# Kernel tuning notes

Measured on AMD Instinct MI355X. Metric: run time of the kernel, lower is better.

## Reference

```python
import jax, jax.numpy as jnp
import numpy as np

D = 256
H1, H2 = 256, 128

def setup_inputs() -> dict:
    key0 = jax.random.key(0)
    ks = jax.random.split(key0, 10)
    B, Lq, Lk = 2, 512, 512
    query = jax.random.normal(ks[0], (B, Lq, D), dtype=jnp.float32)
    key_t = jax.random.normal(ks[1], (B, Lk, D), dtype=jnp.float32)
    value = jax.random.normal(ks[2], (B, Lk, D), dtype=jnp.float32)
    mask = jnp.ones((B, Lq, Lk), dtype=jnp.int32)
    s1 = 1.0 / np.sqrt(2 * D)
    W1 = jax.random.uniform(ks[3], (2 * D, H1), jnp.float32, -s1, s1)  # torch Linear(2D,H1), [in,out]
    b1 = jax.random.uniform(ks[4], (H1,), jnp.float32, -s1, s1)
    s2 = 1.0 / np.sqrt(H1)
    W2 = jax.random.uniform(ks[5], (H1, H2), jnp.float32, -s2, s2)
    b2 = jax.random.uniform(ks[6], (H2,), jnp.float32, -s2, s2)
    s3 = 1.0 / np.sqrt(H2)
    W3 = jax.random.uniform(ks[7], (H2, 1), jnp.float32, -s3, s3)
    b3 = jax.random.uniform(ks[8], (1,), jnp.float32, -s3, s3)
    return {"query": query, "key": key_t, "value": value, "mask": mask,
            "W1": W1, "b1": b1, "W2": W2, "b2": b2, "W3": W3, "b3": b3}

def reference(query, key, value, mask, W1, b1, W2, b2, W3, b3):
    # Original: cat([q_i, k_j]) @ W1 == q_i @ W1[:D] + k_j @ W1[D:]  (algebraic split,
    # identical math, avoids materializing the [B,Lq,Lk,2D] concat tensor).
    W1q, W1k = W1[:D], W1[D:]
    qp = jnp.einsum('bqd,dh->bqh', query, W1q)           # [B,Lq,H1]
    kp = jnp.einsum('bkd,dh->bkh', key, W1k)             # [B,Lk,H1]
    h1 = jax.nn.relu(qp[:, :, None, :] + kp[:, None, :, :] + b1)   # [B,Lq,Lk,H1]
    h2 = jax.nn.relu(jnp.einsum('bqkh,hj->bqkj', h1, W2) + b2)      # [B,Lq,Lk,H2]
    scores = (jnp.einsum('bqkj,jo->bqko', h2, W3) + b3)[..., 0]     # [B,Lq,Lk]
    scores = jnp.where(mask == 0, jnp.float32(-1e9), scores)
    attn = jax.nn.softmax(scores, axis=-1)               # dropout is identity in eval mode
    out = jnp.einsum('bqk,bkd->bqd', attn, value)
    return out, attn
```

## Files before the change

### kernel.cpp

```cpp
#include <hip/hip_runtime.h>

#define D_  256
#define H1_ 256
#define H2_ 128
#define B_  2
#define LQ_ 512
#define LK_ 512
#define BK  64

typedef float  f32x4  __attribute__((ext_vector_type(4)));
typedef __bf16 bf16x8 __attribute__((ext_vector_type(8)));
typedef __bf16 bf16x4 __attribute__((ext_vector_type(4)));

__global__ __launch_bounds__(512) void prep_kernel(
    const float* __restrict__ query, const float* __restrict__ key,
    const float* __restrict__ W1, const float* __restrict__ b1,
    const float* __restrict__ W2,
    float* __restrict__ qp, float* __restrict__ kp, __bf16* __restrict__ w2t) {
  const int blk = blockIdx.x;
  const int tid = threadIdx.x;
  if (blk >= 256) {
    const int id = (blk - 256) * 512 + tid;
    const int n = id >> 8;
    const int k = id & 255;
    w2t[n * H1_ + k] = (__bf16)W2[k * H2_ + n];
    return;
  }
  __shared__ float in_lds[8][D_];
  __shared__ float part[8][H1_];
  const int row0 = blk * 8;
  const int sel  = row0 >> 10;
  const float* __restrict__ src = sel ? key : query;
  const int base = (row0 & 1023) * D_;
  for (int i = tid; i < 8 * D_; i += 512)
    in_lds[i >> 8][i & 255] = src[base + i];
  __syncthreads();
  const int h  = tid & 255;
  const int kh = tid >> 8;
  float acc[8] = {0.f, 0.f, 0.f, 0.f, 0.f, 0.f, 0.f, 0.f};
  const float* __restrict__ w = W1 + sel * D_ * H1_ + kh * 128 * H1_ + h;
#pragma unroll 4
  for (int dd = 0; dd < 128; ++dd) {
    const float wv = w[dd * H1_];
    const int d = kh * 128 + dd;
#pragma unroll
    for (int r = 0; r < 8; ++r) acc[r] += in_lds[r][d] * wv;
  }
  if (kh == 1) {
#pragma unroll
    for (int r = 0; r < 8; ++r) part[r][h] = acc[r];
  }
  __syncthreads();
  if (kh == 0) {
    const float bias = sel ? 0.0f : b1[h];
    float* __restrict__ dst = sel ? kp : qp;
#pragma unroll
    for (int r = 0; r < 8; ++r)
      dst[base + r * H1_ + h] = acc[r] + part[r][h] + bias;
  }
}

__global__ __launch_bounds__(256, 2) void score_kernel(
    const float* __restrict__ qp, const float* __restrict__ kp,
    const __bf16* __restrict__ w2t,
    const float* __restrict__ b2, const float* __restrict__ W3,
    const float* __restrict__ b3, float* __restrict__ scores) {
  __shared__ __bf16 A_lds[128][BK + 8];
  __shared__ __bf16 B_lds[128][BK + 8];
  __shared__ float  spart[2][128];

  const int b  = blockIdx.z;
  const int q0 = blockIdx.y * 8;
  const int k0 = blockIdx.x * 16;
  const int tid  = threadIdx.x;
  const int wave = tid >> 6;
  const int lane = tid & 63;
  const int quad = lane >> 4;
  const int l16  = lane & 15;
  const int wm   = wave >> 1;
  const int wn   = wave & 1;

  const float* __restrict__ qpb = qp + (b * LQ_ + q0) * H1_;
  const float* __restrict__ kpb = kp + (b * LK_ + k0) * H1_;

  f32x4 acc[4][4];
#pragma unroll
  for (int mt = 0; mt < 4; ++mt)
#pragma unroll
    for (int nt = 0; nt < 4; ++nt)
      acc[mt][nt] = (f32x4){0.f, 0.f, 0.f, 0.f};

  for (int kc = 0; kc < H1_ / BK; ++kc) {
#pragma unroll
    for (int i = 0; i < 8; ++i) {
      const int r  = i * 16 + (tid >> 4);
      const int kg = tid & 15;
      const int qi = r >> 4, ki = r & 15;
      const int kcol = kc * BK + kg * 4;
      const float4 qv = *(const float4*)(qpb + qi * H1_ + kcol);
      const float4 kv = *(const float4*)(kpb + ki * H1_ + kcol);
      bf16x4 a;
      a[0] = (__bf16)fmaxf(qv.x + kv.x, 0.f);
      a[1] = (__bf16)fmaxf(qv.y + kv.y, 0.f);
      a[2] = (__bf16)fmaxf(qv.z + kv.z, 0.f);
      a[3] = (__bf16)fmaxf(qv.w + kv.w, 0.f);
      *(bf16x4*)(&A_lds[r][kg * 4]) = a;
    }
#pragma unroll
    for (int i = 0; i < 4; ++i) {
      const int u = i * 256 + tid;
      const int n = u >> 3, seg = u & 7;
      *(uint4*)(&B_lds[n][seg * 8]) =
          *(const uint4*)(w2t + n * H1_ + kc * BK + seg * 8);
    }
    __syncthreads();
#pragma unroll
    for (int ks = 0; ks < BK / 32; ++ks) {
      bf16x8 af[4], bfr[4];
#pragma unroll
      for (int mt = 0; mt < 4; ++mt)
        af[mt] = *(const bf16x8*)(&A_lds[wm * 64 + mt * 16 + l16][ks * 32 + quad * 8]);
#pragma unroll
      for (int nt = 0; nt < 4; ++nt)
        bfr[nt] = *(const bf16x8*)(&B_lds[wn * 64 + nt * 16 + l16][ks * 32 + quad * 8]);
#pragma unroll
      for (int mt = 0; mt < 4; ++mt)
#pragma unroll
        for (int nt = 0; nt < 4; ++nt)
          acc[mt][nt] = __builtin_amdgcn_mfma_f32_16x16x32_bf16(
              af[mt], bfr[nt], acc[mt][nt], 0, 0, 0);
    }
    __syncthreads();
  }

  float part[4][4];
#pragma unroll
  for (int mt = 0; mt < 4; ++mt)
#pragma unroll
    for (int rg = 0; rg < 4; ++rg) part[mt][rg] = 0.f;
#pragma unroll
  for (int nt = 0; nt < 4; ++nt) {
    const int col = wn * 64 + nt * 16 + l16;
    const float b2v = b2[col];
    const float w3v = W3[col];
#pragma unroll
    for (int mt = 0; mt < 4; ++mt)
#pragma unroll
      for (int rg = 0; rg < 4; ++rg) {
        float h2 = acc[mt][nt][rg] + b2v;
        h2 = fmaxf(h2, 0.f);
        part[mt][rg] += h2 * w3v;
      }
  }
#pragma unroll
  for (int off = 1; off < 16; off <<= 1)
#pragma unroll
    for (int mt = 0; mt < 4; ++mt)
#pragma unroll
      for (int rg = 0; rg < 4; ++rg)
        part[mt][rg] += __shfl_xor(part[mt][rg], off, 64);
  if (l16 == 0) {
#pragma unroll
    for (int mt = 0; mt < 4; ++mt)
#pragma unroll
      for (int rg = 0; rg < 4; ++rg) {
        const int rl = wm * 64 + mt * 16 + quad * 4 + rg;
        spart[wn][rl] = part[mt][rg];
      }
  }
  __syncthreads();
  if (tid < 128) {
    const float s = spart[0][tid] + spart[1][tid] + b3[0];
    const int qi = tid >> 4, ki = tid & 15;
    scores[(b * LQ_ + q0 + qi) * LK_ + k0 + ki] = s;
  }
}

__global__ void softmax_kernel(float* __restrict__ attn,
                               const int* __restrict__ mask) {
  const int row = blockIdx.x;
  const int tid = threadIdx.x;
  __shared__ float redm[4];
  __shared__ float reds[4];
  float* __restrict__ arow = attn + row * LK_;
  const int* __restrict__ mrow = mask + row * LK_;
  float s0 = arow[tid], s1 = arow[tid + 256];
  if (mrow[tid] == 0)       s0 = -1e9f;
  if (mrow[tid + 256] == 0) s1 = -1e9f;
  float m = fmaxf(s0, s1);
#pragma unroll
  for (int off = 32; off; off >>= 1) m = fmaxf(m, __shfl_xor(m, off, 64));
  if ((tid & 63) == 0) redm[tid >> 6] = m;
  __syncthreads();
  m = fmaxf(fmaxf(redm[0], redm[1]), fmaxf(redm[2], redm[3]));
  const float e0 = __expf(s0 - m), e1 = __expf(s1 - m);
  float sum = e0 + e1;
#pragma unroll
  for (int off = 32; off; off >>= 1) sum += __shfl_xor(sum, off, 64);
  if ((tid & 63) == 0) reds[tid >> 6] = sum;
  __syncthreads();
  sum = reds[0] + reds[1] + reds[2] + reds[3];
  const float inv = 1.f / sum;
  arow[tid]       = e0 * inv;
  arow[tid + 256] = e1 * inv;
}

__global__ __launch_bounds__(512) void out_kernel2(
    const float* __restrict__ attn, const float* __restrict__ value,
    float* __restrict__ out) {
  const int ds = blockIdx.x, qg = blockIdx.y, b = blockIdx.z;
  const int tid = threadIdx.x;
  __shared__ float a_lds[8][LK_];
  __shared__ float p_lds[3][8][128];
  const float* __restrict__ abase = attn + (b * LQ_ + qg * 8) * LK_;
  for (int i = tid; i < 8 * LK_; i += 512)
    a_lds[i >> 9][i & 511] = abase[i];
  __syncthreads();
  const int dl = tid & 127;
  const int d  = dl + ds * 128;
  const int kh = tid >> 7;
  float acc[8] = {0.f, 0.f, 0.f, 0.f, 0.f, 0.f, 0.f, 0.f};
  const float* __restrict__ vb = value + (b * LK_ + kh * 128) * D_ + d;
#pragma unroll 4
  for (int k = 0; k < 128; ++k) {
    const float v = vb[k * D_];
    const float* __restrict__ ar = &a_lds[0][kh * 128 + k];
#pragma unroll
    for (int q = 0; q < 8; ++q) acc[q] += ar[q * LK_] * v;
  }
  if (kh > 0) {
#pragma unroll
    for (int q = 0; q < 8; ++q) p_lds[kh - 1][q][dl] = acc[q];
  }
  __syncthreads();
  if (kh == 0) {
    float* __restrict__ ob = out + (b * LQ_ + qg * 8) * D_ + d;
#pragma unroll
    for (int q = 0; q < 8; ++q)
      ob[q * D_] = acc[q] + p_lds[0][q][dl] + p_lds[1][q][dl] + p_lds[2][q][dl];
  }
}

extern "C" void kernel_launch(void* const* d_in, const int* in_sizes, int n_in,
                              void* d_out, int out_size, void* d_ws, size_t ws_size,
                              hipStream_t stream) {
  (void)in_sizes; (void)n_in; (void)out_size; (void)ws_size;
  const float* query = (const float*)d_in[0];
  const float* key   = (const float*)d_in[1];
  const float* value = (const float*)d_in[2];
  const int*   mask  = (const int*)d_in[3];
  const float* W1    = (const float*)d_in[4];
  const float* b1    = (const float*)d_in[5];
  const float* W2    = (const float*)d_in[6];
  const float* b2    = (const float*)d_in[7];
  const float* W3    = (const float*)d_in[8];
  const float* b3    = (const float*)d_in[9];

  float* out  = (float*)d_out;
  float* attn = out + B_ * LQ_ * D_;

  float*  qp  = (float*)d_ws;
  float*  kp  = qp + B_ * LQ_ * H1_;
  __bf16* w2t = (__bf16*)(kp + B_ * LK_ * H1_);

  prep_kernel<<<320, 512, 0, stream>>>(query, key, W1, b1, W2, qp, kp, w2t);
  dim3 gscore(LK_ / 16, LQ_ / 8, B_);
  score_kernel<<<gscore, 256, 0, stream>>>(qp, kp, w2t, b2, W3, b3, attn);
  softmax_kernel<<<B_ * LQ_, 256, 0, stream>>>(attn, mask);
  out_kernel2<<<dim3(2, 64, B_), 512, 0, stream>>>(attn, value, out);
}
```

Before: 154.8 us.

## Swizzle score-kernel LDS layout, raise occupancy, fuse softmax with output GEMV

```diff
diff --git a/kernel.cpp b/kernel.cpp
--- a/kernel.cpp
+++ b/kernel.cpp
@@ -60,13 +60,13 @@
   }
 }
 
-__global__ __launch_bounds__(256, 2) void score_kernel(
+__global__ __launch_bounds__(256, 4) void score_kernel(
     const float* __restrict__ qp, const float* __restrict__ kp,
     const __bf16* __restrict__ w2t,
     const float* __restrict__ b2, const float* __restrict__ W3,
     const float* __restrict__ b3, float* __restrict__ scores) {
-  __shared__ __bf16 A_lds[128][BK + 8];
-  __shared__ __bf16 B_lds[128][BK + 8];
+  __shared__ __align__(16) __bf16 A_lds[128 * BK];
+  __shared__ __align__(16) __bf16 B_lds[128 * BK];
   __shared__ float  spart[2][128];
 
   const int b  = blockIdx.z;
@@ -79,6 +79,7 @@
   const int l16  = lane & 15;
   const int wm   = wave >> 1;
   const int wn   = wave & 1;
+  const int h8   = l16 & 7;
 
   const float* __restrict__ qpb = qp + (b * LQ_ + q0) * H1_;
   const float* __restrict__ kpb = kp + (b * LK_ + k0) * H1_;
@@ -104,25 +105,31 @@
       a[1] = (__bf16)fmaxf(qv.y + kv.y, 0.f);
       a[2] = (__bf16)fmaxf(qv.z + kv.z, 0.f);
       a[3] = (__bf16)fmaxf(qv.w + kv.w, 0.f);
-      *(bf16x4*)(&A_lds[r][kg * 4]) = a;
+      const int sw = (((kg >> 1) ^ (r & 7)) << 3) + ((kg & 1) << 2);
+      *(bf16x4*)(&A_lds[r * BK + sw]) = a;
     }
 #pragma unroll
     for (int i = 0; i < 4; ++i) {
       const int u = i * 256 + tid;
-      const int n = u >> 3, seg = u & 7;
-      *(uint4*)(&B_lds[n][seg * 8]) =
-          *(const uint4*)(w2t + n * H1_ + kc * BK + seg * 8);
+      const int n = u >> 3, c = u & 7;
+      *(uint4*)(&B_lds[n * BK + (((c ^ (n & 7)) << 3))]) =
+          *(const uint4*)(w2t + n * H1_ + kc * BK + c * 8);
     }
     __syncthreads();
 #pragma unroll
     for (int ks = 0; ks < BK / 32; ++ks) {
+      const int cbase = ks * 4 + quad;
       bf16x8 af[4], bfr[4];
 #pragma unroll
-      for (int mt = 0; mt < 4; ++mt)
-        af[mt] = *(const bf16x8*)(&A_lds[wm * 64 + mt * 16 + l16][ks * 32 + quad * 8]);
-#pragma unroll
-      for (int nt = 0; nt < 4; ++nt)
-        bfr[nt] = *(const bf16x8*)(&B_lds[wn * 64 + nt * 16 + l16][ks * 32 + quad * 8]);
+      for (int mt = 0; mt < 4; ++mt) {
+        const int ra = wm * 64 + mt * 16 + l16;
+        af[mt] = *(const bf16x8*)(&A_lds[ra * BK + ((cbase ^ h8) << 3)]);
+      }
+#pragma unroll
+      for (int nt = 0; nt < 4; ++nt) {
+        const int rb = wn * 64 + nt * 16 + l16;
+        bfr[nt] = *(const bf16x8*)(&B_lds[rb * BK + ((cbase ^ h8) << 3)]);
+      }
 #pragma unroll
       for (int mt = 0; mt < 4; ++mt)
 #pragma unroll
@@ -176,68 +183,61 @@
   }
 }
 
-__global__ void softmax_kernel(float* __restrict__ attn,
-                               const int* __restrict__ mask) {
-  const int row = blockIdx.x;
-  const int tid = threadIdx.x;
-  __shared__ float redm[4];
-  __shared__ float reds[4];
-  float* __restrict__ arow = attn + row * LK_;
-  const int* __restrict__ mrow = mask + row * LK_;
-  float s0 = arow[tid], s1 = arow[tid + 256];
-  if (mrow[tid] == 0)       s0 = -1e9f;
-  if (mrow[tid + 256] == 0) s1 = -1e9f;
-  float m = fmaxf(s0, s1);
-#pragma unroll
-  for (int off = 32; off; off >>= 1) m = fmaxf(m, __shfl_xor(m, off, 64));
-  if ((tid & 63) == 0) redm[tid >> 6] = m;
-  __syncthreads();
-  m = fmaxf(fmaxf(redm[0], redm[1]), fmaxf(redm[2], redm[3]));
-  const float e0 = __expf(s0 - m), e1 = __expf(s1 - m);
-  float sum = e0 + e1;
-#pragma unroll
-  for (int off = 32; off; off >>= 1) sum += __shfl_xor(sum, off, 64);
-  if ((tid & 63) == 0) reds[tid >> 6] = sum;
-  __syncthreads();
-  sum = reds[0] + reds[1] + reds[2] + reds[3];
-  const float inv = 1.f / sum;
-  arow[tid]       = e0 * inv;
-  arow[tid + 256] = e1 * inv;
-}
-
-__global__ __launch_bounds__(512) void out_kernel2(
-    const float* __restrict__ attn, const float* __restrict__ value,
-    float* __restrict__ out) {
-  const int ds = blockIdx.x, qg = blockIdx.y, b = blockIdx.z;
+__global__ __launch_bounds__(512) void smout_kernel(
+    float* __restrict__ attn, const int* __restrict__ mask,
+    const float* __restrict__ value, float* __restrict__ out) {
+  const int qg = blockIdx.x, b = blockIdx.y;
   const int tid = threadIdx.x;
   __shared__ float a_lds[8][LK_];
-  __shared__ float p_lds[3][8][128];
-  const float* __restrict__ abase = attn + (b * LQ_ + qg * 8) * LK_;
-  for (int i = tid; i < 8 * LK_; i += 512)
-    a_lds[i >> 9][i & 511] = abase[i];
-  __syncthreads();
-  const int dl = tid & 127;
-  const int d  = dl + ds * 128;
-  const int kh = tid >> 7;
+  __shared__ float p_lds[8][D_];
+  const int row0 = b * LQ_ + qg * 8;
+  const int w = tid >> 6, lane = tid & 63;
+  float* __restrict__ srow = attn + (row0 + w) * LK_;
+  const int* __restrict__ mrow = mask + (row0 + w) * LK_;
+  float v[8];
+#pragma unroll
+  for (int j = 0; j < 8; ++j) {
+    float s = srow[lane + j * 64];
+    if (mrow[lane + j * 64] == 0) s = -1e9f;
+    v[j] = s;
+  }
+  float m = v[0];
+#pragma unroll
+  for (int j = 1; j < 8; ++j) m = fmaxf(m, v[j]);
+#pragma unroll
+  for (int off = 32; off; off >>= 1) m = fmaxf(m, __shfl_xor(m, off, 64));
+  float sum = 0.f;
+#pragma unroll
+  for (int j = 0; j < 8; ++j) { v[j] = __expf(v[j] - m); sum += v[j]; }
+#pragma unroll
+  for (int off = 32; off; off >>= 1) sum += __shfl_xor(sum, off, 64);
+  const float inv = 1.f / sum;
+#pragma unroll
+  for (int j = 0; j < 8; ++j) {
+    const float p = v[j] * inv;
+    a_lds[w][lane + j * 64] = p;
+    srow[lane + j * 64] = p;
+  }
+  __syncthreads();
+  const int d = tid & 255, kh = tid >> 8;
   float acc[8] = {0.f, 0.f, 0.f, 0.f, 0.f, 0.f, 0.f, 0.f};
-  const float* __restrict__ vb = value + (b * LK_ + kh * 128) * D_ + d;
+  const float* __restrict__ vb = value + (b * LK_ + kh * 256) * D_ + d;
 #pragma unroll 4
-  for (int k = 0; k < 128; ++k) {
-    const float v = vb[k * D_];
-    const float* __restrict__ ar = &a_lds[0][kh * 128 + k];
-#pragma unroll
-    for (int q = 0; q < 8; ++q) acc[q] += ar[q * LK_] * v;
-  }
-  if (kh > 0) {
-#pragma unroll
-    for (int q = 0; q < 8; ++q) p_lds[kh - 1][q][dl] = acc[q];
+  for (int k = 0; k < 256; ++k) {
+    const float vv = vb[k * D_];
+    const float* __restrict__ ar = &a_lds[0][kh * 256 + k];
+#pragma unroll
+    for (int q = 0; q < 8; ++q) acc[q] += ar[q * LK_] * vv;
+  }
+  if (kh == 1) {
+#pragma unroll
+    for (int q = 0; q < 8; ++q) p_lds[q][d] = acc[q];
   }
   __syncthreads();
   if (kh == 0) {
-    float* __restrict__ ob = out + (b * LQ_ + qg * 8) * D_ + d;
-#pragma unroll
-    for (int q = 0; q < 8; ++q)
-      ob[q * D_] = acc[q] + p_lds[0][q][dl] + p_lds[1][q][dl] + p_lds[2][q][dl];
+    float* __restrict__ ob = out + row0 * D_ + d;
+#pragma unroll
+    for (int q = 0; q < 8; ++q) ob[q * D_] = acc[q] + p_lds[q][d];
   }
 }
 
@@ -266,6 +266,5 @@
   prep_kernel<<<320, 512, 0, stream>>>(query, key, W1, b1, W2, qp, kp, w2t);
   dim3 gscore(LK_ / 16, LQ_ / 8, B_);
   score_kernel<<<gscore, 256, 0, stream>>>(qp, kp, w2t, b2, W3, b3, attn);
-  softmax_kernel<<<B_ * LQ_, 256, 0, stream>>>(attn, mask);
-  out_kernel2<<<dim3(2, 64, B_), 512, 0, stream>>>(attn, value, out);
-}
+  smout_kernel<<<dim3(64, B_), 512, 0, stream>>>(attn, mask, value, out);
+}
```

New measurement: 167.3 us. +8.1%, slower.
